# Kernel optimization log

Measured on AMD Instinct MI355X. Metric: run time of the kernel, lower is better.

The kernel has to match this reference:

```python
import jax, jax.numpy as jnp
import numpy as np

KS = (0.8, 0.75, 0.667, 0.5)  # pools 500 -> 400 -> 300 -> 200 -> 100 nodes


def gcn(g, h, W, b):
    # torch GCN.forward with p=0: relu(linear(g @ h))
    return jax.nn.relu(jnp.matmul(g, h) @ W.T + b)


def norm_g(g):
    # faithful to torch: [n,n] / [n] broadcasts over the LAST axis (column-normalize)
    return g / jnp.sum(g, axis=1)


def top_k_graph(scores, g, h, k):
    n = g.shape[0]
    kk = max(2, int(k * n))
    values, idx = jax.lax.top_k(scores, kk)  # sorted descending, matches torch.topk
    new_h = h[idx, :] * values[:, None]
    un_g = (g != 0).astype(g.dtype)
    un_g = (jnp.matmul(un_g, un_g) != 0).astype(g.dtype)  # 2-hop connectivity
    un_g = un_g[idx][:, idx]
    return norm_g(un_g), new_h, idx


def setup_inputs() -> dict:
    key = jax.random.key(0)
    ks = jax.random.split(key, 16)
    N, IN_DIM = 500, 32768
    g = (jax.random.uniform(ks[0], (N, N)) < 0.1).astype(jnp.float32)
    h = jax.random.normal(ks[1], (N, IN_DIM), dtype=jnp.float32)
    inp = {
        "g": g,
        "h": h,
        "W_top": jax.random.normal(ks[2], (1, IN_DIM), dtype=jnp.float32) / np.float32(np.sqrt(IN_DIM)),
        "b_top": jnp.zeros((1,), jnp.float32),
    }
    down_dims = [400, 300, 200, 100]
    for i in range(4):
        inp[f"Wp{i}"] = jax.random.normal(ks[3 + i], (1, 1), dtype=jnp.float32)
        inp[f"bp{i}"] = jnp.zeros((1,), jnp.float32)
        inp[f"Wd{i}"] = jax.random.normal(ks[8 + i], (1, down_dims[i]), dtype=jnp.float32) / np.float32(np.sqrt(down_dims[i]))
        inp[f"bd{i}"] = jnp.zeros((1,), jnp.float32)
    return inp


def reference(g, h, W_top, b_top, Wp0, bp0, Wd0, bd0, Wp1, bp1, Wd1, bd1,
              Wp2, bp2, Wd2, bd2, Wp3, bp3, Wd3, bd3):
    Wp = [Wp0, Wp1, Wp2, Wp3]
    bp = [bp0, bp1, bp2, bp3]
    Wd = [Wd0, Wd1, Wd2, Wd3]
    bd = [bd0, bd1, bd2, bd3]
    h = gcn(g, h, W_top, b_top)  # [500, 1]
    h1 = h
    for i in range(4):
        # SAGPool: scores from a tiny GCN(1 -> 1), then topk prune + 2-hop adjacency
        scores = jax.nn.sigmoid(jnp.squeeze(gcn(g, h, Wp[i], bp[i])))  # [n]
        g, h, idx = top_k_graph(scores, g, h, KS[i])
        # down GCN consumes the diagonal matrix built from the pooled 1-feature h
        h = gcn(g, jnp.diag(jnp.squeeze(h)), Wd[i], bd[i])  # [n_i, 1]
        h1 = jnp.concatenate([h1, h], axis=0)
    return h1  # [500+400+300+200+100, 1] = [1500, 1]
```

## Files before the change

kernel.cpp:

```cpp
#include <hip/hip_runtime.h>


#define MS 16
struct P4 { const float* p[4]; };

__device__ __forceinline__ float bitselF(unsigned m, int k, float v) {
    int s = ((int)(m << (31 - k))) >> 31;
    return __int_as_float(s & __float_as_int(v));
}
__device__ __forceinline__ float fbfly(float v) {
#pragma unroll
    for (int o = 32; o; o >>= 1) v += __shfl_xor(v, o);
    return v;
}
__device__ __forceinline__ int ibfly(int v) {
#pragma unroll
    for (int o = 32; o; o >>= 1) v += __shfl_xor(v, o);
    return v;
}
__device__ __forceinline__ float sigm(float x) { return 1.f / (1.f + expf(-x)); }

__device__ __forceinline__ float pwalk16(const unsigned* __restrict__ row,
                                         const float* __restrict__ val) {
    float a = 0.f;
#pragma unroll
    for (int w = 0; w < 16; ++w) {
        unsigned m = row[w];
        while (m) {
            int b = __ffs((int)m) - 1;
            m &= m - 1;
            a += val[(w << 5) + b];
        }
    }
    return a;
}

__device__ __forceinline__ int wrank(const float* __restrict__ sc, float my,
                                     int r, int lane) {
    int cnt = 0;
#pragma unroll
    for (int q = 0; q < 8; ++q) {
        int j = lane + 64 * q;
        float s = sc[j];
        cnt += (s > my) || (s == my && j < r);
    }
    return ibfly(cnt);
}

__global__ __launch_bounds__(1024) void k_dot(const float* __restrict__ h,
        const float* __restrict__ Wt, const float* __restrict__ g,
        float* __restrict__ V, unsigned* __restrict__ MA) {
    int row = blockIdx.x, t = threadIdx.x;
    const float4* h4 = (const float4*)(h + (size_t)row * 32768);
    const float4* w4 = (const float4*)Wt;
    float acc = 0.f;
#pragma unroll
    for (int j = 0; j < 8; ++j) {
        float4 a = h4[t + 1024 * j], b = w4[t + 1024 * j];
        acc = fmaf(a.x, b.x, fmaf(a.y, b.y, fmaf(a.z, b.z, fmaf(a.w, b.w, acc))));
    }
    acc = fbfly(acc);
    __shared__ float red[16];
    if ((t & 63) == 0) red[t >> 6] = acc;
    __syncthreads();
    if (t == 0) {
        float s = 0.f;
        for (int i = 0; i < 16; ++i) s += red[i];
        V[row] = s;
    }
    if (t < 512) {
        float gv = (t < 500) ? g[row * 500 + t] : 0.f;
        unsigned long long bal = __ballot(gv != 0.f);
        if ((t & 63) == 0) {
            int w = t >> 6;
            MA[row * MS + 2 * w] = (unsigned)bal;
            MA[row * MS + 2 * w + 1] = (unsigned)(bal >> 32);
        }
    }
}

__global__ __launch_bounds__(256) void k_row(const unsigned* __restrict__ MA,
        const float* __restrict__ x, const float* __restrict__ c0,
        const float* __restrict__ c1, float* __restrict__ y,
        float* __restrict__ out, int mode) {
    __shared__ float sv[512];
    int t = threadIdx.x;
    sv[t] = (t < 500) ? x[t] : 0.f;
    int t2 = t + 256;
    sv[t2] = (t2 < 500) ? x[t2] : 0.f;
    __syncthreads();
    int wid = t >> 6, lane = t & 63;
    int r = blockIdx.x * 4 + wid;
    float acc = 0.f;
#pragma unroll
    for (int j = 0; j < 8; ++j) {
        unsigned m = MA[r * MS + 2 * j + (lane >> 5)];
        acc += bitselF(m, lane & 31, sv[64 * j + lane]);
    }
    acc = fbfly(acc);
    if (lane == 0) {
        if (mode == 0) {
            float hv = fmaxf(acc + c0[0], 0.f);
            out[r] = hv;
            y[r] = hv;
        } else {
            y[r] = fmaxf(acc * c0[0] + c1[0], 0.f);
        }
    }
}

__global__ __launch_bounds__(256) void k_rh(const unsigned* __restrict__ MA,
        const float* __restrict__ SHg, const float* __restrict__ Zg,
        int* __restrict__ IDXA, float* __restrict__ HSo,
        unsigned* __restrict__ CPP) {
    __shared__ __align__(16) unsigned sMA[8000];
    __shared__ float sz[512];
    int t = threadIdx.x, wid = t >> 6, lane = t & 63;
    for (int q = t; q < 2000; q += 256)
        ((uint4*)sMA)[q] = ((const uint4*)MA)[q];
    if (t < 500) sz[t] = Zg[t];
    else if (t < 512) sz[t] = -1.f;
    int t2 = t + 256;
    if (t2 < 500) sz[t2] = Zg[t2];
    else if (t2 < 512) sz[t2] = -1.f;
    __syncthreads();
    int i = blockIdx.x * 4 + wid;
    float my = sz[i];
    int rank = wrank(sz, my, i, lane);
    if (rank >= 400) return;
    if (lane == 0) {
        IDXA[rank] = i;
        HSo[i] = SHg[i] * sigm(my);
    }
    int part = lane >> 4, w = lane & 15;
    unsigned acc = 0;
    for (int k = part; k < 500; k += 4) {
        unsigned sel = (sMA[i * MS + (k >> 5)] >> (k & 31)) & 1u;
        acc |= sMA[k * MS + w] & (0u - sel);
    }
    acc |= (unsigned)__shfl_xor((int)acc, 16);
    acc |= (unsigned)__shfl_xor((int)acc, 32);
    if (lane < 16) {
        unsigned m500 = (lane < 15) ? 0xffffffffu : 0xfffffu;
        CPP[i * MS + lane] = ~acc & m500;
    }
}

__global__ __launch_bounds__(1024) void k_fin(const int* __restrict__ IDXA,
        const unsigned* __restrict__ CPP, const float* __restrict__ HSo,
        P4 Wp, P4 bp, P4 Wd, P4 bd, float* __restrict__ out) {
    __shared__ __align__(16) unsigned sCP[8000];
    __shared__ float szC[512], svC[512], s2C[512];
    __shared__ float svO[512], s2O[512], shvO[512], sHSo[512], srsO[512];
    __shared__ int sIDXp[2][512];
    __shared__ unsigned sSELp[2][16];
    __shared__ float sS[8];
    __shared__ float stot0, stot1, stotS;
    __shared__ int sFlag;
    int t = threadIdx.x, wid = t >> 6, lane = t & 63;
    if (t < 512) sIDXp[0][t] = (t < 400) ? IDXA[t] : 0;
    if (t < 16) {
        sSELp[0][t] = 0u;
        sSELp[1][t] = 0u;
    }
    if (t == 0) sFlag = 0;
    __syncthreads();
    if (t < 400) {
        int i = sIDXp[0][t];
        atomicOr(&sSELp[0][i >> 5], 1u << (i & 31));
    }
    __syncthreads();
    for (int q = t; q < 6400; q += 1024) {
        int c = q >> 4, w = q & 15;
        int i = sIDXp[0][c];
        sCP[i * MS + w] = CPP[i * MS + w] & sSELp[0][w];
    }
    __syncthreads();
    if (t < 400) {
        int i = sIDXp[0][t];
        int pc = 0;
#pragma unroll
        for (int w = 0; w < 16; ++w) pc += __popc(sCP[i * MS + w]);
        float rs = (float)(400 - pc);
        srsO[i] = rs;
        float su = HSo[i] * Wd.p[0][t] / rs;
        svC[t] = su;
        svO[i] = su;
    } else if (t < 512) {
        svC[t] = 0.f;
    }
    __syncthreads();
    if (t < 64) {
        float p = 0.f;
#pragma unroll
        for (int j = 0; j < 8; ++j) p += svC[t * 8 + j];
        p = fbfly(p);
        if (t == 0) stot0 = p;
    }
    __syncthreads();
    int i0 = 0;
    if (t < 400) {
        i0 = sIDXp[0][t];
        float corr = pwalk16(sCP + i0 * MS, svO);
        float h1 = fmaxf(stot0 - corr + bd.p[0][0], 0.f);
        out[500 + t] = h1;
        shvO[i0] = h1;
        float s2 = h1 / srsO[i0];
        s2C[t] = s2;
        s2O[i0] = s2;
    } else if (t < 512) {
        s2C[t] = 0.f;
    }
    __syncthreads();
    if (t < 64) {
        float p = 0.f;
#pragma unroll
        for (int j = 0; j < 8; ++j) p += s2C[t * 8 + j];
        p = fbfly(p);
        if (t == 0) stot1 = p;
    }
    __syncthreads();
    if (t < 400) {
        float c2 = pwalk16(sCP + i0 * MS, s2O);
        szC[t] = fmaxf((stot1 - c2) * Wp.p[1][0] + bp.p[1][0], 0.f);
    } else if (t < 512) {
        szC[t] = -1.f;
    }
    __syncthreads();
    for (int r0 = wid * 2; r0 < 400; r0 += 32) {
        int r1 = r0 + 1;
        float my0 = szC[r0], my1 = szC[r1];
        int cnt = 0;
#pragma unroll
        for (int q = 0; q < 8; ++q) {
            int j = lane + 64 * q;
            float s = szC[j];
            cnt += (s > my0) || (s == my0 && j < r0);
            cnt += ((s > my1) || (s == my1 && j < r1)) << 16;
        }
        cnt = ibfly(cnt);
        if (lane == 0) {
            int c0 = cnt & 0xffff, c1 = cnt >> 16;
            if (c0 < 300) {
                int io = sIDXp[0][r0];
                sIDXp[1][c0] = io;
                sHSo[io] = shvO[io] * sigm(my0);
                atomicOr(&sSELp[1][io >> 5], 1u << (io & 31));
            }
            if (c1 < 300) {
                int io = sIDXp[0][r1];
                sIDXp[1][c1] = io;
                sHSo[io] = shvO[io] * sigm(my1);
                atomicOr(&sSELp[1][io >> 5], 1u << (io & 31));
            }
        }
    }
    __syncthreads();
    unsigned P[16];
    int inew = 0, pc = 0;
    float su_ = 0.f;
    if (t < 300) {
        inew = sIDXp[1][t];
#pragma unroll
        for (int w = 0; w < 16; ++w) P[w] = sSELp[1][w];
        bool alive = true;
        for (int w2 = 0; w2 < 16 && alive; ++w2) {
            unsigned nb = sSELp[0][w2] & ~sCP[inew * MS + w2];
            while (nb) {
                int b = __ffs((int)nb) - 1;
                nb &= nb - 1;
                const unsigned* cj = sCP + (w2 * 32 + b) * MS;
                unsigned orr = 0;
#pragma unroll
                for (int w = 0; w < 16; ++w) {
                    P[w] &= cj[w];
                    orr |= P[w];
                }
                if (!orr) { alive = false; break; }
            }
        }
#pragma unroll
        for (int w = 0; w < 16; ++w) pc += __popc(P[w]);
        if (pc > 0) atomicOr(&sFlag, 1);
        float rs = (float)(300 - pc);
        su_ = sHSo[inew] * Wd.p[1][t] / rs;
    }
    __syncthreads();
    if (t < 300) {
#pragma unroll
        for (int w = 0; w < 16; ++w) sCP[inew * MS + w] = P[w];
        srsO[inew] = (float)(300 - pc);
        svC[t] = su_;
        svO[inew] = su_;
    } else if (t < 512) {
        svC[t] = 0.f;
    }
    __syncthreads();
    if (sFlag == 0) {
        if (t < 64) {
            float p = 0.f;
#pragma unroll
            for (int j = 0; j < 8; ++j) p += svC[t * 8 + j];
            p = fbfly(p);
            if (t == 0) {
                float h2 = fmaxf(p + bd.p[1][0], 0.f);
                float z2 = fmaxf(h2 * Wp.p[2][0] + bp.p[2][0], 0.f);
                sS[0] = h2;
                sS[1] = h2 * sigm(z2);
            }
        }
        __syncthreads();
        float HS2 = sS[1];
        if (t < 512) s2C[t] = (t < 200) ? HS2 * Wd.p[2][t] / 200.f : 0.f;
        __syncthreads();
        if (t < 64) {
            float p = 0.f;
#pragma unroll
            for (int j = 0; j < 8; ++j) p += s2C[t * 8 + j];
            p = fbfly(p);
            if (t == 0) {
                float h3 = fmaxf(p + bd.p[2][0], 0.f);
                float z3 = fmaxf(h3 * Wp.p[3][0] + bp.p[3][0], 0.f);
                sS[2] = h3;
                sS[3] = h3 * sigm(z3);
            }
        }
        __syncthreads();
        float HS3 = sS[3];
        if (t < 512) s2C[t] = (t < 100) ? HS3 * Wd.p[3][t] / 100.f : 0.f;
        __syncthreads();
        if (t < 64) {
            float p = 0.f;
#pragma unroll
            for (int j = 0; j < 8; ++j) p += s2C[t * 8 + j];
            p = fbfly(p);
            if (t == 0) sS[4] = fmaxf(p + bd.p[3][0], 0.f);
        }
        __syncthreads();
        if (t < 300) out[900 + t] = sS[0];
        else if (t < 500) out[1200 + (t - 300)] = sS[2];
        else if (t < 600) out[1400 + (t - 500)] = sS[4];
        return;
    }
    const int kks[3] = {300, 200, 100};
    const int kns[3] = {200, 100, 0};
    const int offs[3] = {900, 1200, 1400};
    for (int l = 1; l <= 3; ++l) {
        const int kk = kks[l - 1], knext = kns[l - 1], off = offs[l - 1];
        const int cur = l & 1, nxt = cur ^ 1;
        if (t < 64) {
            float p = 0.f;
#pragma unroll
            for (int j = 0; j < 8; ++j) p += svC[t * 8 + j];
            p = fbfly(p);
            if (t == 0) stotS = p;
        }
        __syncthreads();
        int i_ = 0;
        if (t < kk) {
            i_ = sIDXp[cur][t];
            float corr = pwalk16(sCP + i_ * MS, svO);
            float hv = fmaxf(stotS - corr + bd.p[l][0], 0.f);
            out[off + t] = hv;
            shvO[i_] = hv;
            float s2 = hv / srsO[i_];
            s2C[t] = s2;
            s2O[i_] = s2;
        } else if (t < 512) {
            s2C[t] = 0.f;
        }
        if (l == 3) break;
        __syncthreads();
        if (t < 64) {
            float p = 0.f;
#pragma unroll
            for (int j = 0; j < 8; ++j) p += s2C[t * 8 + j];
            p = fbfly(p);
            if (t == 0) stotS = p;
        }
        if (t < 16) sSELp[nxt][t] = 0u;
        __syncthreads();
        float z_ = -1.f;
        if (t < kk) {
            float c2 = pwalk16(sCP + i_ * MS, s2O);
            z_ = fmaxf((stotS - c2) * Wp.p[l + 1][0] + bp.p[l + 1][0], 0.f);
        }
        if (t < 512) szC[t] = (t < kk) ? z_ : -1.f;
        __syncthreads();
        for (int r = wid; r < kk; r += 16) {
            float my = szC[r];
            int cnt = wrank(szC, my, r, lane);
            if (lane == 0 && cnt < knext) {
                int io = sIDXp[cur][r];
                sIDXp[nxt][cnt] = io;
                sHSo[io] = shvO[io] * sigm(my);
                atomicOr(&sSELp[nxt][io >> 5], 1u << (io & 31));
            }
        }
        __syncthreads();
        unsigned Q[16];
        int in2 = 0, pc2 = 0;
        float su2_ = 0.f;
        if (t < knext) {
            in2 = sIDXp[nxt][t];
#pragma unroll
            for (int w = 0; w < 16; ++w) Q[w] = sSELp[nxt][w];
            bool alive = true;
            for (int w2 = 0; w2 < 16 && alive; ++w2) {
                unsigned nb = sSELp[cur][w2] & ~sCP[in2 * MS + w2];
                while (nb) {
                    int b = __ffs((int)nb) - 1;
                    nb &= nb - 1;
                    const unsigned* cj = sCP + (w2 * 32 + b) * MS;
                    unsigned orr = 0;
#pragma unroll
                    for (int w = 0; w < 16; ++w) {
                        Q[w] &= cj[w];
                        orr |= Q[w];
                    }
                    if (!orr) { alive = false; break; }
                }
            }
#pragma unroll
            for (int w = 0; w < 16; ++w) pc2 += __popc(Q[w]);
            float rs = (float)(knext - pc2);
            su2_ = sHSo[in2] * Wd.p[l + 1][t] / rs;
        }
        __syncthreads();
        if (t < knext) {
#pragma unroll
            for (int w = 0; w < 16; ++w) sCP[in2 * MS + w] = Q[w];
            srsO[in2] = (float)(knext - pc2);
            svC[t] = su2_;
            svO[in2] = su2_;
        } else if (t < 512) {
            svC[t] = 0.f;
        }
        __syncthreads();
    }
}

extern "C" void kernel_launch(void* const* d_in, const int* in_sizes, int n_in,
                              void* d_out, int out_size, void* d_ws, size_t ws_size,
                              hipStream_t stream) {
    const float* g = (const float*)d_in[0];
    const float* h = (const float*)d_in[1];
    const float* W_top = (const float*)d_in[2];
    const float* b_top = (const float*)d_in[3];
    P4 Wp, bp, Wd, bd;
    for (int i = 0; i < 4; ++i) {
        Wp.p[i] = (const float*)d_in[4 + 4 * i];
        bp.p[i] = (const float*)d_in[5 + 4 * i];
        Wd.p[i] = (const float*)d_in[6 + 4 * i];
        bd.p[i] = (const float*)d_in[7 + 4 * i];
    }
    float* out = (float*)d_out;

    unsigned* wsu = (unsigned*)d_ws;
    float* V = (float*)(wsu + 0);
    float* SHg = (float*)(wsu + 512);
    float* Zg = (float*)(wsu + 1024);
    int* IDXA = (int*)(wsu + 1536);
    float* HSo = (float*)(wsu + 2048);
    unsigned* CPP = wsu + 2560;
    unsigned* MA = wsu + 10560;

    k_dot<<<500, 1024, 0, stream>>>(h, W_top, g, V, MA);
    k_row<<<125, 256, 0, stream>>>(MA, V, b_top, nullptr, SHg, out, 0);
    k_row<<<125, 256, 0, stream>>>(MA, SHg, Wp.p[0], bp.p[0], Zg, nullptr, 1);
    k_rh<<<125, 256, 0, stream>>>(MA, SHg, Zg, IDXA, HSo, CPP);
    k_fin<<<1, 1024, 0, stream>>>(IDXA, CPP, HSo, Wp, bp, Wd, bd, out);
}
```

Before: 55.85 us.

## Fuse two row GCN kernels into one by recomputing neighbor activations

The two back-to-back k_row launches (first GCN layer, then pooling score layer) are merged into a single k_shz kernel. Each block copies the whole bitmask adjacency into shared memory and, for each row, builds a neighbor list with ballots. It then recomputes each neighbor's first-layer activation instead of waiting for a grid-wide write. This removes one kernel launch and its global round trip, at the cost of redundant per-neighbor work. In k_fin, the full CPP matrix is now bulk-copied into shared memory and selected bits are counted with a per-bit loop, replacing the masked gather pass and one sync.

```diff
diff --git a/kernel.cpp b/kernel.cpp
--- a/kernel.cpp
+++ b/kernel.cpp
@@ -79,34 +79,53 @@
     }
 }
 
-__global__ __launch_bounds__(256) void k_row(const unsigned* __restrict__ MA,
-        const float* __restrict__ x, const float* __restrict__ c0,
-        const float* __restrict__ c1, float* __restrict__ y,
-        float* __restrict__ out, int mode) {
+__global__ __launch_bounds__(256) void k_shz(const unsigned* __restrict__ MA,
+        const float* __restrict__ V, const float* __restrict__ b_top,
+        const float* __restrict__ Wp0, const float* __restrict__ bp0,
+        float* __restrict__ SHg, float* __restrict__ Zg,
+        float* __restrict__ out) {
+    __shared__ __align__(16) unsigned sMA[8000];
     __shared__ float sv[512];
-    int t = threadIdx.x;
-    sv[t] = (t < 500) ? x[t] : 0.f;
+    __shared__ int nlist[4][512];
+    int t = threadIdx.x, wid = t >> 6, lane = t & 63;
+    for (int q = t; q < 2000; q += 256)
+        ((uint4*)sMA)[q] = ((const uint4*)MA)[q];
+    sv[t] = (t < 500) ? V[t] : 0.f;
     int t2 = t + 256;
-    sv[t2] = (t2 < 500) ? x[t2] : 0.f;
-    __syncthreads();
-    int wid = t >> 6, lane = t & 63;
-    int r = blockIdx.x * 4 + wid;
+    sv[t2] = (t2 < 500) ? V[t2] : 0.f;
+    __syncthreads();
+    int i = blockIdx.x * 4 + wid;
     float acc = 0.f;
 #pragma unroll
     for (int j = 0; j < 8; ++j) {
-        unsigned m = MA[r * MS + 2 * j + (lane >> 5)];
+        unsigned m = sMA[i * MS + 2 * j + (lane >> 5)];
         acc += bitselF(m, lane & 31, sv[64 * j + lane]);
     }
     acc = fbfly(acc);
+    float shi = fmaxf(acc + b_top[0], 0.f);
     if (lane == 0) {
-        if (mode == 0) {
-            float hv = fmaxf(acc + c0[0], 0.f);
-            out[r] = hv;
-            y[r] = hv;
-        } else {
-            y[r] = fmaxf(acc * c0[0] + c1[0], 0.f);
-        }
-    }
+        out[i] = shi;
+        SHg[i] = shi;
+    }
+    int base = 0;
+#pragma unroll
+    for (int q = 0; q < 8; ++q) {
+        unsigned mw = sMA[i * MS + 2 * q + (lane >> 5)];
+        int has = (mw >> (lane & 31)) & 1;
+        unsigned long long bal = __ballot(has);
+        int pre = (int)__popcll(bal & ((1ull << lane) - 1ull));
+        if (has) nlist[wid][base + pre] = 64 * q + lane;
+        base += (int)__popcll(bal);
+    }
+    __builtin_amdgcn_wave_barrier();
+    float zacc = 0.f;
+    for (int p = lane; p < base; p += 64) {
+        int j = nlist[wid][p];
+        float a = pwalk16(sMA + j * MS, sv);
+        zacc += fmaxf(a + b_top[0], 0.f);
+    }
+    zacc = fbfly(zacc);
+    if (lane == 0) Zg[i] = fmaxf(zacc * Wp0[0] + bp0[0], 0.f);
 }
 
 __global__ __launch_bounds__(256) void k_rh(const unsigned* __restrict__ MA,
@@ -158,7 +177,15 @@
     __shared__ float stot0, stot1, stotS;
     __shared__ int sFlag;
     int t = threadIdx.x, wid = t >> 6, lane = t & 63;
-    if (t < 512) sIDXp[0][t] = (t < 400) ? IDXA[t] : 0;
+    for (int q = t; q < 2000; q += 1024)
+        ((uint4*)sCP)[q] = ((const uint4*)CPP)[q];
+    if (t < 512) {
+        sIDXp[0][t] = (t < 400) ? IDXA[t] : 0;
+        svO[t] = 0.f;
+        s2O[t] = 0.f;
+        svC[t] = 0.f;
+        srsO[t] = 1.f;
+    }
     if (t < 16) {
         sSELp[0][t] = 0u;
         sSELp[1][t] = 0u;
@@ -170,24 +197,24 @@
         atomicOr(&sSELp[0][i >> 5], 1u << (i & 31));
     }
     __syncthreads();
-    for (int q = t; q < 6400; q += 1024) {
-        int c = q >> 4, w = q & 15;
-        int i = sIDXp[0][c];
-        sCP[i * MS + w] = CPP[i * MS + w] & sSELp[0][w];
-    }
-    __syncthreads();
     if (t < 400) {
         int i = sIDXp[0][t];
-        int pc = 0;
-#pragma unroll
-        for (int w = 0; w < 16; ++w) pc += __popc(sCP[i * MS + w]);
-        float rs = (float)(400 - pc);
+        int cnt = 0;
+#pragma unroll
+        for (int w = 0; w < 16; ++w) {
+            unsigned m = sCP[i * MS + w];
+            unsigned sw = sSELp[0][w];
+            while (m) {
+                int b = __ffs((int)m) - 1;
+                m &= m - 1;
+                cnt += (sw >> b) & 1;
+            }
+        }
+        float rs = (float)(400 - cnt);
         srsO[i] = rs;
         float su = HSo[i] * Wd.p[0][t] / rs;
         svC[t] = su;
         svO[i] = su;
-    } else if (t < 512) {
-        svC[t] = 0.f;
     }
     __syncthreads();
     if (t < 64) {
@@ -466,8 +493,7 @@
     unsigned* MA = wsu + 10560;
 
     k_dot<<<500, 1024, 0, stream>>>(h, W_top, g, V, MA);
-    k_row<<<125, 256, 0, stream>>>(MA, V, b_top, nullptr, SHg, out, 0);
-    k_row<<<125, 256, 0, stream>>>(MA, SHg, Wp.p[0], bp.p[0], Zg, nullptr, 1);
+    k_shz<<<125, 256, 0, stream>>>(MA, V, b_top, Wp.p[0], bp.p[0], SHg, Zg, out);
     k_rh<<<125, 256, 0, stream>>>(MA, SHg, Zg, IDXA, HSo, CPP);
     k_fin<<<1, 1024, 0, stream>>>(IDXA, CPP, HSo, Wp, bp, Wd, bd, out);
 }
```

After: 67.14 us. 20.2% more time.
